# Optimization experiments

Hardware: AMD Instinct MI355X
Metric: run time of the kernel (lower is better)

The kernel has to match this reference:

```python
import jax, jax.numpy as jnp
import numpy as np

N, E, NFEAT, NHID, NCLASS = 40000, 640000, 128, 128, 40
LN_EPS = 1e-5
L2_EPS = 1e-12


def layer_norm(x, g, b):
    mu = jnp.mean(x, axis=-1, keepdims=True)
    var = jnp.var(x, axis=-1, keepdims=True)
    return (x - mu) * jax.lax.rsqrt(var + LN_EPS) * g + b


def gcn_conv(x, edge_index, edge_weight, Wl, bl, Wr):
    # lin_l projection then PyG propagate (gather src, weight, scatter-add dst)
    h = x @ Wl.T + bl                                  # [N, out]
    msg = h[edge_index[0]] * edge_weight[:, None]       # [E, out]
    agg = jax.ops.segment_sum(msg, edge_index[1], num_segments=N)
    out = agg + x @ Wr.T                                # root (lin_r, no bias)
    # F.normalize(p=2, dim=-1)
    nrm = jnp.sqrt(jnp.sum(out * out, axis=-1, keepdims=True))
    return out / jnp.maximum(nrm, L2_EPS)


def setup_inputs() -> dict:
    key = jax.random.key(0)
    ks = jax.random.split(key, 12)
    x = jax.random.normal(ks[0], (N, NFEAT), dtype=jnp.float32)
    edge_index = jax.random.randint(ks[1], (2, E), 0, N, dtype=jnp.int64)
    edge_weight = jax.random.uniform(ks[2], (E,), dtype=jnp.float32)
    # kaiming-normal-ish init scales
    s0 = np.sqrt(2.0 / NFEAT)
    s1 = np.sqrt(2.0 / NHID)
    return {
        "x": x,
        "edge_index": edge_index,
        "edge_weight": edge_weight,
        "ln0_g": jnp.ones((NFEAT,), jnp.float32),
        "ln0_b": jnp.zeros((NFEAT,), jnp.float32),
        "W0l": jax.random.normal(ks[3], (NHID, NFEAT), jnp.float32) * s0,
        "b0l": jnp.zeros((NHID,), jnp.float32),
        "W0r": jax.random.normal(ks[4], (NHID, NFEAT), jnp.float32) * s0,
        "ln1_g": jnp.ones((NHID,), jnp.float32),
        "ln1_b": jnp.zeros((NHID,), jnp.float32),
        "W1l": jax.random.normal(ks[5], (NCLASS, NHID), jnp.float32) * s1,
        "b1l": jnp.zeros((NCLASS,), jnp.float32),
        "W1r": jax.random.normal(ks[6], (NCLASS, NHID), jnp.float32) * s1,
    }


def reference(x, edge_index, edge_weight, ln0_g, ln0_b, W0l, b0l, W0r,
              ln1_g, ln1_b, W1l, b1l, W1r):
    # layer_norm_first
    h = layer_norm(x, ln0_g, ln0_b)
    h = gcn_conv(h, edge_index, edge_weight, W0l, b0l, W0r)
    h = layer_norm(h, ln1_g, ln1_b)
    h = jax.nn.relu(h)  # dropout inactive in eval mode
    h = gcn_conv(h, edge_index, edge_weight, W1l, b1l, W1r)
    return jax.nn.log_softmax(h, axis=1)
```

## Files before the change

kernel.cpp:

```cpp
#include <hip/hip_runtime.h>
#include <math.h>

#define N_NODES 40000
#define N_EDGES 640000
#define BCAP 64
#define FGRP 8
#define FRANGE (N_NODES / FGRP)
#define NSG 1271

typedef __attribute__((ext_vector_type(8))) short short8;
typedef __attribute__((ext_vector_type(4))) float f32x4;

__device__ __forceinline__ unsigned short f2bf(float f) {
    union { float f; unsigned u; } v; v.f = f;
    unsigned r = (v.u + 0x7FFFu + ((v.u >> 16) & 1u)) >> 16;
    return (unsigned short)r;
}
__device__ __forceinline__ float bf2f(unsigned short h) {
    union { unsigned u; float f; } v; v.u = ((unsigned)h) << 16;
    return v.f;
}

__device__ __forceinline__ float wave_sum(float v) {
    #pragma unroll
    for (int m = 1; m < 64; m <<= 1) v += __shfl_xor(v, m, 64);
    return v;
}
__device__ __forceinline__ float wave_max(float v) {
    #pragma unroll
    for (int m = 1; m < 64; m <<= 1) v = fmaxf(v, __shfl_xor(v, m, 64));
    return v;
}

__global__ __launch_bounds__(256) void comboFill_kernel(const float* __restrict__ x,
        const float* __restrict__ g, const float* __restrict__ b,
        unsigned short* __restrict__ h0h, unsigned short* __restrict__ h0l,
        const float* __restrict__ W0l, const float* __restrict__ W0r,
        const float* __restrict__ W1l, const float* __restrict__ W1r,
        unsigned short* __restrict__ Wt1h, unsigned short* __restrict__ Wt1l,
        unsigned short* __restrict__ Wt2h, unsigned short* __restrict__ Wt2l,
        const int* __restrict__ ei, const float* __restrict__ ew,
        int* __restrict__ cnt, unsigned int* __restrict__ sPk) {
    int bid = blockIdx.x;
    int phase = bid % 24;
    if (phase < 8) {
        int cb = (bid / 24) * 8 + phase;
        if (cb < 10000) {
            int row = cb * 4 + (threadIdx.x >> 6);
            int lane = threadIdx.x & 63;
            float2 v = ((const float2*)(x + (size_t)row * 128))[lane];
            float mu = wave_sum(v.x + v.y) * (1.0f / 128.0f);
            float dx = v.x - mu, dy = v.y - mu;
            float var = wave_sum(dx * dx + dy * dy) * (1.0f / 128.0f);
            float rs = rsqrtf(var + 1e-5f);
            float2 gv = ((const float2*)g)[lane];
            float2 bv = ((const float2*)b)[lane];
            float ox = dx * rs * gv.x + bv.x;
            float oy = dy * rs * gv.y + bv.y;
            ushort2 hv, lv;
            hv.x = f2bf(ox); hv.y = f2bf(oy);
            lv.x = f2bf(ox - bf2f(hv.x)); lv.y = f2bf(oy - bf2f(hv.y));
            ((ushort2*)(h0h + (size_t)row * 128))[lane] = hv;
            ((ushort2*)(h0l + (size_t)row * 128))[lane] = lv;
        } else {
            int i = (cb - 10000) * 256 + threadIdx.x;
            float w; unsigned short *ph, *pl; int idx;
            if (i < 256 * 128) {
                int c = i >> 7, k = i & 127;
                w = (c < 128) ? W0l[c * 128 + k] : W0r[(c - 128) * 128 + k];
                ph = Wt1h; pl = Wt1l; idx = i;
            } else {
                int j = i - 256 * 128;
                int c = j >> 7, k = j & 127;
                w = (c < 40) ? W1l[c * 128 + k] : W1r[(c - 40) * 128 + k];
                ph = Wt2h; pl = Wt2l; idx = j;
            }
            unsigned short hi = f2bf(w);
            ph[idx] = hi;
            pl[idx] = f2bf(w - bf2f(hi));
        }
    } else {
        int gp = bid & 7;
        int chunk = (bid / 24) * 2 + ((phase - 8) >> 3);
        if (chunk < N_EDGES / 256) {
            int e = chunk * 256 + threadIdx.x;
            int d = ei[N_EDGES + e];
            int lo = gp * FRANGE;
            if (d >= lo && d < lo + FRANGE) {
                unsigned int pk = (unsigned int)ei[e] | ((unsigned int)f2bf(ew[e]) << 16);
                int rank = atomicAdd(&cnt[d], 1);
                if (rank < BCAP) sPk[(size_t)d * BCAP + rank] = pk;
            }
        }
    }
}


__global__ __launch_bounds__(256) void gemm1_kernel(
        const unsigned short* __restrict__ h0h, const unsigned short* __restrict__ h0l,
        const unsigned short* __restrict__ Wt1h, const unsigned short* __restrict__ Wt1l,
        const float* __restrict__ b0l,
        unsigned short* __restrict__ hl, float* __restrict__ agg) {
    __shared__ unsigned short Bs[2][128 * 128];
    int tid = threadIdx.x;
    int cBase = blockIdx.y * 128;
    #pragma unroll
    for (int plane = 0; plane < 2; ++plane) {
        const unsigned short* src = plane ? Wt1l : Wt1h;
        char* dst = (char*)Bs[plane];
        #pragma unroll
        for (int i = 0; i < 8; ++i) {
            int gid = i * 256 + tid;
            int c = gid >> 4, kc = gid & 15;
            short8 v = *(const short8*)(src + (size_t)(cBase + c) * 128 + kc * 8);
            int byte = (c * 256 + kc * 16) ^ ((c & 7) << 4);
            *(short8*)(dst + byte) = v;
        }
    }
    __syncthreads();

    int wid = tid >> 6, lane = tid & 63;
    int rBase = (blockIdx.x * 4 + wid) * 32;
    if (rBase < N_NODES) {
        int lr = lane & 15;
        int lk = (lane >> 4) * 8;
        int sw = (lr & 7) << 4;
        const unsigned short* a0h = h0h + (size_t)(rBase + lr) * 128 + lk;
        const unsigned short* a0l = h0l + (size_t)(rBase + lr) * 128 + lk;
        const unsigned short* a1h = a0h + 16 * 128;
        const unsigned short* a1l = a0l + 16 * 128;
        f32x4 acc[2][8] = {};
        #pragma unroll
        for (int ks = 0; ks < 4; ++ks) {
            int kb = ks * 32;
            short8 A0h = *(const short8*)(a0h + kb);
            short8 A0l = *(const short8*)(a0l + kb);
            short8 A1h = *(const short8*)(a1h + kb);
            short8 A1l = *(const short8*)(a1l + kb);
            #pragma unroll
            for (int ct = 0; ct < 8; ++ct) {
                int bb = (((ct * 16 + lr) << 8) + (ks << 6) + ((lane >> 4) << 4)) ^ sw;
                short8 Bh = *(const short8*)((const char*)Bs[0] + bb);
                short8 Bl = *(const short8*)((const char*)Bs[1] + bb);
                acc[0][ct] = __builtin_amdgcn_mfma_f32_16x16x32_bf16(A0h, Bh, acc[0][ct], 0, 0, 0);
                acc[0][ct] = __builtin_amdgcn_mfma_f32_16x16x32_bf16(A0h, Bl, acc[0][ct], 0, 0, 0);
                acc[0][ct] = __builtin_amdgcn_mfma_f32_16x16x32_bf16(A0l, Bh, acc[0][ct], 0, 0, 0);
                acc[1][ct] = __builtin_amdgcn_mfma_f32_16x16x32_bf16(A1h, Bh, acc[1][ct], 0, 0, 0);
                acc[1][ct] = __builtin_amdgcn_mfma_f32_16x16x32_bf16(A1h, Bl, acc[1][ct], 0, 0, 0);
                acc[1][ct] = __builtin_amdgcn_mfma_f32_16x16x32_bf16(A1l, Bh, acc[1][ct], 0, 0, 0);
            }
        }
        int orow = (lane >> 4) * 4;
        #pragma unroll
        for (int rt = 0; rt < 2; ++rt) {
            int row = rBase + rt * 16 + orow;
            #pragma unroll
            for (int ct = 0; ct < 8; ++ct) {
                int col = cBase + ct * 16 + lr;
                if (col < 128) {
                    float bias = b0l[col];
                    #pragma unroll
                    for (int j = 0; j < 4; ++j)
                        hl[(size_t)(row + j) * 128 + col] = f2bf(acc[rt][ct][j] + bias);
                } else {
                    int cc = col - 128;
                    #pragma unroll
                    for (int j = 0; j < 4; ++j)
                        agg[(size_t)(row + j) * 128 + cc] = acc[rt][ct][j];
                }
            }
        }
    }
}

__global__ __launch_bounds__(256) void gemm2_kernel(
        const unsigned short* __restrict__ h2h, const unsigned short* __restrict__ h2l,
        const unsigned short* __restrict__ Wt2h, const unsigned short* __restrict__ Wt2l,
        const float* __restrict__ b1l,
        unsigned short* __restrict__ gl, float* __restrict__ agg2) {
    __shared__ unsigned short Bs[2][80 * 128];
    int tid = threadIdx.x;
    #pragma unroll
    for (int plane = 0; plane < 2; ++plane) {
        const unsigned short* src = plane ? Wt2l : Wt2h;
        char* dst = (char*)Bs[plane];
        #pragma unroll
        for (int i = 0; i < 5; ++i) {
            int gid = i * 256 + tid;
            int c = gid >> 4, kc = gid & 15;
            short8 v = *(const short8*)(src + (size_t)c * 128 + kc * 8);
            int byte = (c * 256 + kc * 16) ^ ((c & 7) << 4);
            *(short8*)(dst + byte) = v;
        }
    }
    __syncthreads();

    int wid = tid >> 6, lane = tid & 63;
    int rBase = (blockIdx.x * 4 + wid) * 32;
    if (rBase < N_NODES) {
        int lr = lane & 15;
        int lk = (lane >> 4) * 8;
        int sw = (lr & 7) << 4;
        const unsigned short* a0h = h2h + (size_t)(rBase + lr) * 128 + lk;
        const unsigned short* a0l = h2l + (size_t)(rBase + lr) * 128 + lk;
        const unsigned short* a1h = a0h + 16 * 128;
        const unsigned short* a1l = a0l + 16 * 128;
        f32x4 acc[2][5] = {};
        #pragma unroll
        for (int ks = 0; ks < 4; ++ks) {
            int kb = ks * 32;
            short8 A0h = *(const short8*)(a0h + kb);
            short8 A0l = *(const short8*)(a0l + kb);
            short8 A1h = *(const short8*)(a1h + kb);
            short8 A1l = *(const short8*)(a1l + kb);
            #pragma unroll
            for (int ct = 0; ct < 5; ++ct) {
                int bb = (((ct * 16 + lr) << 8) + (ks << 6) + ((lane >> 4) << 4)) ^ sw;
                short8 Bh = *(const short8*)((const char*)Bs[0] + bb);
                short8 Bl = *(const short8*)((const char*)Bs[1] + bb);
                acc[0][ct] = __builtin_amdgcn_mfma_f32_16x16x32_bf16(A0h, Bh, acc[0][ct], 0, 0, 0);
                acc[0][ct] = __builtin_amdgcn_mfma_f32_16x16x32_bf16(A0h, Bl, acc[0][ct], 0, 0, 0);
                acc[0][ct] = __builtin_amdgcn_mfma_f32_16x16x32_bf16(A0l, Bh, acc[0][ct], 0, 0, 0);
                acc[1][ct] = __builtin_amdgcn_mfma_f32_16x16x32_bf16(A1h, Bh, acc[1][ct], 0, 0, 0);
                acc[1][ct] = __builtin_amdgcn_mfma_f32_16x16x32_bf16(A1h, Bl, acc[1][ct], 0, 0, 0);
                acc[1][ct] = __builtin_amdgcn_mfma_f32_16x16x32_bf16(A1l, Bh, acc[1][ct], 0, 0, 0);
            }
        }
        int orow = (lane >> 4) * 4;
        #pragma unroll
        for (int rt = 0; rt < 2; ++rt) {
            int row = rBase + rt * 16 + orow;
            #pragma unroll
            for (int ct = 0; ct < 5; ++ct) {
                int col = ct * 16 + lr;
                if (col < 40) {
                    float bias = b1l[col];
                    #pragma unroll
                    for (int j = 0; j < 4; ++j)
                        gl[(size_t)(row + j) * 40 + col] = f2bf(acc[rt][ct][j] + bias);
                } else {
                    int cc = col - 40;
                    #pragma unroll
                    for (int j = 0; j < 4; ++j)
                        agg2[(size_t)(row + j) * 40 + cc] = acc[rt][ct][j];
                }
            }
        }
    }
}

__global__ __launch_bounds__(256) void gather1_kernel(const int* __restrict__ cnt,
        const unsigned int* __restrict__ sPk, const unsigned short* __restrict__ hl,
        const float* __restrict__ agg,
        const float* __restrict__ g, const float* __restrict__ b,
        unsigned short* __restrict__ h2h, unsigned short* __restrict__ h2l) {
    int row = blockIdx.x * 4 + (threadIdx.x >> 6);
    int lane = threadIdx.x & 63;
    int n = cnt[row]; n = n > BCAP ? BCAP : n;
    const unsigned int* ep = sPk + (size_t)row * BCAP;
    float2 acc = ((const float2*)(agg + (size_t)row * 128))[lane];
    int e = 0;
    for (; e + 8 <= n; e += 8) {
        uint4 q0 = *(const uint4*)(ep + e);
        uint4 q1 = *(const uint4*)(ep + e + 4);
        ushort2 u0 = ((const ushort2*)(hl + (size_t)(q0.x & 0xFFFF) * 128))[lane];
        ushort2 u1 = ((const ushort2*)(hl + (size_t)(q0.y & 0xFFFF) * 128))[lane];
        ushort2 u2 = ((const ushort2*)(hl + (size_t)(q0.z & 0xFFFF) * 128))[lane];
        ushort2 u3 = ((const ushort2*)(hl + (size_t)(q0.w & 0xFFFF) * 128))[lane];
        ushort2 u4 = ((const ushort2*)(hl + (size_t)(q1.x & 0xFFFF) * 128))[lane];
        ushort2 u5 = ((const ushort2*)(hl + (size_t)(q1.y & 0xFFFF) * 128))[lane];
        ushort2 u6 = ((const ushort2*)(hl + (size_t)(q1.z & 0xFFFF) * 128))[lane];
        ushort2 u7 = ((const ushort2*)(hl + (size_t)(q1.w & 0xFFFF) * 128))[lane];
        float w0 = bf2f((unsigned short)(q0.x >> 16)), w1 = bf2f((unsigned short)(q0.y >> 16));
        float w2 = bf2f((unsigned short)(q0.z >> 16)), w3 = bf2f((unsigned short)(q0.w >> 16));
        float w4 = bf2f((unsigned short)(q1.x >> 16)), w5 = bf2f((unsigned short)(q1.y >> 16));
        float w6 = bf2f((unsigned short)(q1.z >> 16)), w7 = bf2f((unsigned short)(q1.w >> 16));
        acc.x = fmaf(bf2f(u0.x), w0, acc.x); acc.y = fmaf(bf2f(u0.y), w0, acc.y);
        acc.x = fmaf(bf2f(u1.x), w1, acc.x); acc.y = fmaf(bf2f(u1.y), w1, acc.y);
        acc.x = fmaf(bf2f(u2.x), w2, acc.x); acc.y = fmaf(bf2f(u2.y), w2, acc.y);
        acc.x = fmaf(bf2f(u3.x), w3, acc.x); acc.y = fmaf(bf2f(u3.y), w3, acc.y);
        acc.x = fmaf(bf2f(u4.x), w4, acc.x); acc.y = fmaf(bf2f(u4.y), w4, acc.y);
        acc.x = fmaf(bf2f(u5.x), w5, acc.x); acc.y = fmaf(bf2f(u5.y), w5, acc.y);
        acc.x = fmaf(bf2f(u6.x), w6, acc.x); acc.y = fmaf(bf2f(u6.y), w6, acc.y);
        acc.x = fmaf(bf2f(u7.x), w7, acc.x); acc.y = fmaf(bf2f(u7.y), w7, acc.y);
    }
    for (; e < n; ++e) {
        unsigned int p = ep[e];
        ushort2 u = ((const ushort2*)(hl + (size_t)(p & 0xFFFF) * 128))[lane];
        float w = bf2f((unsigned short)(p >> 16));
        acc.x = fmaf(bf2f(u.x), w, acc.x);
        acc.y = fmaf(bf2f(u.y), w, acc.y);
    }
    float nrm = sqrtf(wave_sum(acc.x * acc.x + acc.y * acc.y));
    float inv = 1.0f / fmaxf(nrm, 1e-12f);
    float vx = acc.x * inv, vy = acc.y * inv;
    float mu = wave_sum(vx + vy) * (1.0f / 128.0f);
    float dx = vx - mu, dy = vy - mu;
    float var = wave_sum(dx * dx + dy * dy) * (1.0f / 128.0f);
    float rs = rsqrtf(var + 1e-5f);
    float2 gv = ((const float2*)g)[lane];
    float2 bv = ((const float2*)b)[lane];
    float ox = fmaxf(dx * rs * gv.x + bv.x, 0.0f);
    float oy = fmaxf(dy * rs * gv.y + bv.y, 0.0f);
    ushort2 hv, lv;
    hv.x = f2bf(ox); hv.y = f2bf(oy);
    lv.x = f2bf(ox - bf2f(hv.x)); lv.y = f2bf(oy - bf2f(hv.y));
    ((ushort2*)(h2h + (size_t)row * 128))[lane] = hv;
    ((ushort2*)(h2l + (size_t)row * 128))[lane] = lv;
}

__global__ __launch_bounds__(256) void gather2_kernel(const int* __restrict__ cnt,
        const unsigned int* __restrict__ sPk, const unsigned short* __restrict__ gl,
        const float* __restrict__ agg2, float* __restrict__ out) {
    int row = blockIdx.x * 4 + (threadIdx.x >> 6);
    int lane = threadIdx.x & 63;
    bool act = lane < 40;
    int n = cnt[row]; n = n > BCAP ? BCAP : n;
    const unsigned int* ep = sPk + (size_t)row * BCAP;
    float acc = act ? agg2[(size_t)row * 40 + lane] : 0.0f;
    int e = 0;
    for (; e + 8 <= n; e += 8) {
        uint4 q0 = *(const uint4*)(ep + e);
        uint4 q1 = *(const uint4*)(ep + e + 4);
        if (act) {
            float v0 = bf2f(gl[(size_t)(q0.x & 0xFFFF) * 40 + lane]);
            float v1 = bf2f(gl[(size_t)(q0.y & 0xFFFF) * 40 + lane]);
            float v2 = bf2f(gl[(size_t)(q0.z & 0xFFFF) * 40 + lane]);
            float v3 = bf2f(gl[(size_t)(q0.w & 0xFFFF) * 40 + lane]);
            float v4 = bf2f(gl[(size_t)(q1.x & 0xFFFF) * 40 + lane]);
            float v5 = bf2f(gl[(size_t)(q1.y & 0xFFFF) * 40 + lane]);
            float v6 = bf2f(gl[(size_t)(q1.z & 0xFFFF) * 40 + lane]);
            float v7 = bf2f(gl[(size_t)(q1.w & 0xFFFF) * 40 + lane]);
            acc = fmaf(v0, bf2f((unsigned short)(q0.x >> 16)), acc);
            acc = fmaf(v1, bf2f((unsigned short)(q0.y >> 16)), acc);
            acc = fmaf(v2, bf2f((unsigned short)(q0.z >> 16)), acc);
            acc = fmaf(v3, bf2f((unsigned short)(q0.w >> 16)), acc);
            acc = fmaf(v4, bf2f((unsigned short)(q1.x >> 16)), acc);
            acc = fmaf(v5, bf2f((unsigned short)(q1.y >> 16)), acc);
            acc = fmaf(v6, bf2f((unsigned short)(q1.z >> 16)), acc);
            acc = fmaf(v7, bf2f((unsigned short)(q1.w >> 16)), acc);
        }
    }
    for (; e < n; ++e) {
        unsigned int p = ep[e];
        if (act) {
            float v = bf2f(gl[(size_t)(p & 0xFFFF) * 40 + lane]);
            acc = fmaf(v, bf2f((unsigned short)(p >> 16)), acc);
        }
    }
    float nrm = sqrtf(wave_sum(act ? acc * acc : 0.0f));
    float o = acc / fmaxf(nrm, 1e-12f);
    float m = wave_max(act ? o : -INFINITY);
    float s = wave_sum(act ? expf(o - m) : 0.0f);
    float ls = logf(s);
    if (act) out[(size_t)row * 40 + lane] = o - m - ls;
}

extern "C" void kernel_launch(void* const* d_in, const int* in_sizes, int n_in,
                              void* d_out, int out_size, void* d_ws, size_t ws_size,
                              hipStream_t stream) {
    const float* x    = (const float*)d_in[0];
    const int*   ei   = (const int*)d_in[1];
    const float* ew   = (const float*)d_in[2];
    const float* ln0g = (const float*)d_in[3];
    const float* ln0b = (const float*)d_in[4];
    const float* W0l  = (const float*)d_in[5];
    const float* b0l  = (const float*)d_in[6];
    const float* W0r  = (const float*)d_in[7];
    const float* ln1g = (const float*)d_in[8];
    const float* ln1b = (const float*)d_in[9];
    const float* W1l  = (const float*)d_in[10];
    const float* b1l  = (const float*)d_in[11];
    const float* W1r  = (const float*)d_in[12];
    float* out = (float*)d_out;

    const size_t NBUF = (size_t)N_NODES * 128;
    char* p = (char*)d_ws;
    auto alloc = [&](size_t bytes) { char* r = p; p += (bytes + 255) & ~(size_t)255; return r; };
    float*          agg  = (float*)alloc(NBUF * 4);
    unsigned short* hl   = (unsigned short*)alloc(NBUF * 2);
    unsigned short* h0h  = (unsigned short*)alloc(NBUF * 2);
    unsigned short* h0l  = (unsigned short*)alloc(NBUF * 2);
    unsigned short* Wt1h = (unsigned short*)alloc(256 * 128 * 2);
    unsigned short* Wt1l = (unsigned short*)alloc(256 * 128 * 2);
    unsigned short* Wt2h = (unsigned short*)alloc(80 * 128 * 2);
    unsigned short* Wt2l = (unsigned short*)alloc(80 * 128 * 2);
    unsigned int*   sPk  = (unsigned int*)alloc((size_t)N_NODES * BCAP * 4);
    int*            cnt  = (int*)alloc(N_NODES * 4);
    unsigned short* gl   = hl;
    float*        agg2   = agg;

    hipMemsetAsync(cnt, 0, (size_t)N_NODES * 4, stream);
    comboFill_kernel<<<NSG * 24, 256, 0, stream>>>(x, ln0g, ln0b, h0h, h0l,
            W0l, W0r, W1l, W1r, Wt1h, Wt1l, Wt2h, Wt2l, ei, ew, cnt, sPk);
    gemm1_kernel<<<dim3(313, 2), 256, 0, stream>>>(h0h, h0l, Wt1h, Wt1l, b0l, hl, agg);
    gather1_kernel<<<N_NODES / 4, 256, 0, stream>>>(cnt, sPk, hl, agg,
                                                    ln1g, ln1b, h0h, h0l);
    gemm2_kernel<<<313, 256, 0, stream>>>(h0h, h0l, Wt2h, Wt2l, b1l, gl, agg2);
    gather2_kernel<<<N_NODES / 4, 256, 0, stream>>>(cnt, sPk, gl, agg2, out);
}
```

Measured before the change: 132.0 us.

## Rebalance fill block mix, halve gemm1 column tile, pad gl row stride

The combined fill kernel now interleaves two layernorm/weight blocks with one edge-bucketing block that handles four 256-edge chunks per dst-range group, replacing the 8-of-24 phase layout. gemm1 now uses 64-column tiles over a 4-wide grid, which halves shared memory and accumulator registers per block to raise occupancy, at the cost of reloading A rows twice as often. The layer-2 projection buffer gl is given a 64-element row stride instead of 40, aligning gathered rows to 128 bytes. This adds padding memory and changes the work balance across blocks.

```diff
diff --git a/kernel.cpp b/kernel.cpp
--- a/kernel.cpp
+++ b/kernel.cpp
@@ -6,7 +6,9 @@
 #define BCAP 64
 #define FGRP 8
 #define FRANGE (N_NODES / FGRP)
-#define NSG 1271
+#define NCHUNK (N_EDGES / 256)
+#define NSG 5084
+#define GLS 64
 
 typedef __attribute__((ext_vector_type(8))) short short8;
 typedef __attribute__((ext_vector_type(4))) float f32x4;
@@ -42,9 +44,9 @@
         const int* __restrict__ ei, const float* __restrict__ ew,
         int* __restrict__ cnt, unsigned int* __restrict__ sPk) {
     int bid = blockIdx.x;
-    int phase = bid % 24;
-    if (phase < 8) {
-        int cb = (bid / 24) * 8 + phase;
+    int ph = bid % 3;
+    if (ph < 2) {
+        int cb = (bid / 3) * 2 + ph;
         if (cb < 10000) {
             int row = cb * 4 + (threadIdx.x >> 6);
             int lane = threadIdx.x & 63;
@@ -64,32 +66,37 @@
             ((ushort2*)(h0l + (size_t)row * 128))[lane] = lv;
         } else {
             int i = (cb - 10000) * 256 + threadIdx.x;
-            float w; unsigned short *ph, *pl; int idx;
+            float w; unsigned short *ph2, *pl; int idx;
             if (i < 256 * 128) {
                 int c = i >> 7, k = i & 127;
                 w = (c < 128) ? W0l[c * 128 + k] : W0r[(c - 128) * 128 + k];
-                ph = Wt1h; pl = Wt1l; idx = i;
+                ph2 = Wt1h; pl = Wt1l; idx = i;
             } else {
                 int j = i - 256 * 128;
                 int c = j >> 7, k = j & 127;
                 w = (c < 40) ? W1l[c * 128 + k] : W1r[(c - 40) * 128 + k];
-                ph = Wt2h; pl = Wt2l; idx = j;
+                ph2 = Wt2h; pl = Wt2l; idx = j;
             }
             unsigned short hi = f2bf(w);
-            ph[idx] = hi;
+            ph2[idx] = hi;
             pl[idx] = f2bf(w - bf2f(hi));
         }
     } else {
         int gp = bid & 7;
-        int chunk = (bid / 24) * 2 + ((phase - 8) >> 3);
-        if (chunk < N_EDGES / 256) {
-            int e = chunk * 256 + threadIdx.x;
-            int d = ei[N_EDGES + e];
-            int lo = gp * FRANGE;
-            if (d >= lo && d < lo + FRANGE) {
-                unsigned int pk = (unsigned int)ei[e] | ((unsigned int)f2bf(ew[e]) << 16);
-                int rank = atomicAdd(&cnt[d], 1);
-                if (rank < BCAP) sPk[(size_t)d * BCAP + rank] = pk;
+        int f = bid / 3;
+        int j = f >> 3;
+        int lo = gp * FRANGE;
+        #pragma unroll
+        for (int cc = 0; cc < 4; ++cc) {
+            int chunk = j * 4 + cc;
+            if (chunk < NCHUNK) {
+                int e = chunk * 256 + threadIdx.x;
+                int d = ei[N_EDGES + e];
+                if (d >= lo && d < lo + FRANGE) {
+                    unsigned int pk = (unsigned int)ei[e] | ((unsigned int)f2bf(ew[e]) << 16);
+                    int rank = atomicAdd(&cnt[d], 1);
+                    if (rank < BCAP) sPk[(size_t)d * BCAP + rank] = pk;
+                }
             }
         }
     }
@@ -101,15 +108,15 @@
         const unsigned short* __restrict__ Wt1h, const unsigned short* __restrict__ Wt1l,
         const float* __restrict__ b0l,
         unsigned short* __restrict__ hl, float* __restrict__ agg) {
-    __shared__ unsigned short Bs[2][128 * 128];
+    __shared__ unsigned short Bs[2][64 * 128];
     int tid = threadIdx.x;
-    int cBase = blockIdx.y * 128;
+    int cBase = blockIdx.y * 64;
     #pragma unroll
     for (int plane = 0; plane < 2; ++plane) {
         const unsigned short* src = plane ? Wt1l : Wt1h;
         char* dst = (char*)Bs[plane];
         #pragma unroll
-        for (int i = 0; i < 8; ++i) {
+        for (int i = 0; i < 4; ++i) {
             int gid = i * 256 + tid;
             int c = gid >> 4, kc = gid & 15;
             short8 v = *(const short8*)(src + (size_t)(cBase + c) * 128 + kc * 8);
@@ -129,7 +136,7 @@
         const unsigned short* a0l = h0l + (size_t)(rBase + lr) * 128 + lk;
         const unsigned short* a1h = a0h + 16 * 128;
         const unsigned short* a1l = a0l + 16 * 128;
-        f32x4 acc[2][8] = {};
+        f32x4 acc[2][4] = {};
         #pragma unroll
         for (int ks = 0; ks < 4; ++ks) {
             int kb = ks * 32;
@@ -138,7 +145,7 @@
             short8 A1h = *(const short8*)(a1h + kb);
             short8 A1l = *(const short8*)(a1l + kb);
             #pragma unroll
-            for (int ct = 0; ct < 8; ++ct) {
+            for (int ct = 0; ct < 4; ++ct) {
                 int bb = (((ct * 16 + lr) << 8) + (ks << 6) + ((lane >> 4) << 4)) ^ sw;
                 short8 Bh = *(const short8*)((const char*)Bs[0] + bb);
                 short8 Bl = *(const short8*)((const char*)Bs[1] + bb);
@@ -155,7 +162,7 @@
         for (int rt = 0; rt < 2; ++rt) {
             int row = rBase + rt * 16 + orow;
             #pragma unroll
-            for (int ct = 0; ct < 8; ++ct) {
+            for (int ct = 0; ct < 4; ++ct) {
                 int col = cBase + ct * 16 + lr;
                 if (col < 128) {
                     float bias = b0l[col];
@@ -237,7 +244,7 @@
                     float bias = b1l[col];
                     #pragma unroll
                     for (int j = 0; j < 4; ++j)
-                        gl[(size_t)(row + j) * 40 + col] = f2bf(acc[rt][ct][j] + bias);
+                        gl[(size_t)(row + j) * GLS + col] = f2bf(acc[rt][ct][j] + bias);
                 } else {
                     int cc = col - 40;
                     #pragma unroll
@@ -323,14 +330,14 @@
         uint4 q0 = *(const uint4*)(ep + e);
         uint4 q1 = *(const uint4*)(ep + e + 4);
         if (act) {
-            float v0 = bf2f(gl[(size_t)(q0.x & 0xFFFF) * 40 + lane]);
-            float v1 = bf2f(gl[(size_t)(q0.y & 0xFFFF) * 40 + lane]);
-            float v2 = bf2f(gl[(size_t)(q0.z & 0xFFFF) * 40 + lane]);
-            float v3 = bf2f(gl[(size_t)(q0.w & 0xFFFF) * 40 + lane]);
-            float v4 = bf2f(gl[(size_t)(q1.x & 0xFFFF) * 40 + lane]);
-            float v5 = bf2f(gl[(size_t)(q1.y & 0xFFFF) * 40 + lane]);
-            float v6 = bf2f(gl[(size_t)(q1.z & 0xFFFF) * 40 + lane]);
-            float v7 = bf2f(gl[(size_t)(q1.w & 0xFFFF) * 40 + lane]);
+            float v0 = bf2f(gl[(size_t)(q0.x & 0xFFFF) * GLS + lane]);
+            float v1 = bf2f(gl[(size_t)(q0.y & 0xFFFF) * GLS + lane]);
+            float v2 = bf2f(gl[(size_t)(q0.z & 0xFFFF) * GLS + lane]);
+            float v3 = bf2f(gl[(size_t)(q0.w & 0xFFFF) * GLS + lane]);
+            float v4 = bf2f(gl[(size_t)(q1.x & 0xFFFF) * GLS + lane]);
+            float v5 = bf2f(gl[(size_t)(q1.y & 0xFFFF) * GLS + lane]);
+            float v6 = bf2f(gl[(size_t)(q1.z & 0xFFFF) * GLS + lane]);
+            float v7 = bf2f(gl[(size_t)(q1.w & 0xFFFF) * GLS + lane]);
             acc = fmaf(v0, bf2f((unsigned short)(q0.x >> 16)), acc);
             acc = fmaf(v1, bf2f((unsigned short)(q0.y >> 16)), acc);
             acc = fmaf(v2, bf2f((unsigned short)(q0.z >> 16)), acc);
@@ -344,7 +351,7 @@
     for (; e < n; ++e) {
         unsigned int p = ep[e];
         if (act) {
-            float v = bf2f(gl[(size_t)(p & 0xFFFF) * 40 + lane]);
+            float v = bf2f(gl[(size_t)(p & 0xFFFF) * GLS + lane]);
             acc = fmaf(v, bf2f((unsigned short)(p >> 16)), acc);
         }
     }
@@ -391,9 +398,9 @@
     float*        agg2   = agg;
 
     hipMemsetAsync(cnt, 0, (size_t)N_NODES * 4, stream);
-    comboFill_kernel<<<NSG * 24, 256, 0, stream>>>(x, ln0g, ln0b, h0h, h0l,
+    comboFill_kernel<<<NSG * 3, 256, 0, stream>>>(x, ln0g, ln0b, h0h, h0l,
             W0l, W0r, W1l, W1r, Wt1h, Wt1l, Wt2h, Wt2l, ei, ew, cnt, sPk);
-    gemm1_kernel<<<dim3(313, 2), 256, 0, stream>>>(h0h, h0l, Wt1h, Wt1l, b0l, hl, agg);
+    gemm1_kernel<<<dim3(313, 4), 256, 0, stream>>>(h0h, h0l, Wt1h, Wt1l, b0l, hl, agg);
     gather1_kernel<<<N_NODES / 4, 256, 0, stream>>>(cnt, sPk, hl, agg,
                                                     ln1g, ln1b, h0h, h0l);
     gemm2_kernel<<<313, 256, 0, stream>>>(h0h, h0l, Wt2h, Wt2l, b1l, gl, agg2);
```

Result: slower. 140.4 us (+6.3%).
